# Performance work log

Hardware: AMD Instinct MI355X
Metric: run time of the kernel (lower is better)

## Reference

```python
import jax, jax.numpy as jnp
import numpy as np
import math

THETA = 1.0


def _qdense(xa, xb, wa, wb, ba, bb):
    # QComplexDense: j_squared = -cos(2*theta)
    j2 = -math.cos(2.0 * THETA)
    out_a = xa @ wa.T + j2 * (xb @ wb.T) + ba
    out_b = xa @ wb.T + xb @ wa.T + bb
    return out_a, out_b


def setup_inputs() -> dict:
    key = jax.random.key(0)
    B, S, D = 4, 2048, 1024
    ks = jax.random.split(key, 16)
    limit = math.sqrt(6.0 / (D + D))  # xavier uniform for square [D,D]

    def w(k):
        return jax.random.uniform(k, (D, D), jnp.float32, -limit, limit)

    inp = {
        'xa': jax.random.normal(ks[0], (B, S, D), jnp.float32),
        'xb': jax.random.normal(ks[1], (B, S, D), jnp.float32),
    }
    i = 2
    for n in ('q', 'k', 'v', 'o'):
        inp[n + '_wa'] = w(ks[i]); inp[n + '_wb'] = w(ks[i + 1])
        inp[n + '_ba'] = jnp.zeros((D,), jnp.float32)
        inp[n + '_bb'] = jnp.zeros((D,), jnp.float32)
        i += 2
    return inp


def reference(xa, xb,
              q_wa, q_wb, q_ba, q_bb,
              k_wa, k_wb, k_ba, k_bb,
              v_wa, v_wb, v_ba, v_bb,
              o_wa, o_wb, o_ba, o_bb):
    D = xa.shape[-1]
    # NOTE: qc_matmul in the original uses cos(2 * ones(1)) == cos(2.0),
    # a constant independent of theta.
    c2 = math.cos(2.0)

    Qa, Qb = _qdense(xa, xb, q_wa, q_wb, q_ba, q_bb)
    Ka, Kb = _qdense(xa, xb, k_wa, k_wb, k_ba, k_bb)
    Va, Vb = _qdense(xa, xb, v_wa, v_wb, v_ba, v_bb)

    # complex-style QK^T: scores_a = Qa Ka^T - cos(2) Qb Kb^T ; scores_b = Qa Kb^T + Qb Ka^T
    sa = jnp.einsum('bsd,btd->bst', Qa, Ka) - c2 * jnp.einsum('bsd,btd->bst', Qb, Kb)
    sb = jnp.einsum('bsd,btd->bst', Qa, Kb) + jnp.einsum('bsd,btd->bst', Qb, Ka)
    scores_real = jnp.sqrt(sa * sa + sb * sb)  # magnitude
    attn = jax.nn.softmax(scores_real / math.sqrt(D), axis=-1)  # [B,S,S]

    out_a = jnp.einsum('bst,btd->bsd', attn, Va)
    out_b = jnp.einsum('bst,btd->bsd', attn, Vb)
    return _qdense(out_a, out_b, o_wa, o_wb, o_ba, o_bb)
```

## Files before the change

### kernel.cpp

```cpp
#include <hip/hip_runtime.h>
#include <math.h>

typedef __bf16 bf16_t;
typedef __attribute__((ext_vector_type(16))) float f32x16;
typedef __attribute__((ext_vector_type(8))) __bf16 v8bf;
typedef __attribute__((ext_vector_type(4))) __bf16 v4bf;

#define GLLDS(g, l)                                                           \
  __builtin_amdgcn_global_load_lds(                                           \
      (const __attribute__((address_space(1))) void*)(g),                     \
      (__attribute__((address_space(3))) void*)(l), 16, 0, 0)
#define OPQ(p) asm volatile("" : "+v"(p))

__global__ void sentinel_kernel(float* o, float v) { o[0] = v; }

__global__ __launch_bounds__(256) void pack_x_kernel(
    const float* __restrict__ xa, const float* __restrict__ xb,
    bf16_t* __restrict__ xcat, int n4)
{
  int i = blockIdx.x * 256 + threadIdx.x;
  if (i >= n4) return;
  float4 a = reinterpret_cast<const float4*>(xa)[i];
  float4 b = reinterpret_cast<const float4*>(xb)[i];
  long e = (long)i * 4;
  long m = e >> 10;
  int  d = (int)(e & 1023);
  v4bf av = { (bf16_t)a.x, (bf16_t)a.y, (bf16_t)a.z, (bf16_t)a.w };
  v4bf bv = { (bf16_t)b.x, (bf16_t)b.y, (bf16_t)b.z, (bf16_t)b.w };
  *reinterpret_cast<v4bf*>(xcat + m * 2048 + d)        = av;
  *reinterpret_cast<v4bf*>(xcat + m * 2048 + 1024 + d) = bv;
}

__global__ __launch_bounds__(256) void pack_w_kernel(
    const float* __restrict__ wa, const float* __restrict__ wb,
    bf16_t* __restrict__ outA, bf16_t* __restrict__ outB, float j2)
{
  int i = blockIdx.x * 256 + threadIdx.x;
  float4 a = reinterpret_cast<const float4*>(wa)[i];
  float4 b = reinterpret_cast<const float4*>(wb)[i];
  long e = (long)i * 4;
  long n = e >> 10;
  int  k = (int)(e & 1023);
  v4bf av = { (bf16_t)a.x, (bf16_t)a.y, (bf16_t)a.z, (bf16_t)a.w };
  v4bf bv = { (bf16_t)b.x, (bf16_t)b.y, (bf16_t)b.z, (bf16_t)b.w };
  v4bf jb = { (bf16_t)(j2*b.x), (bf16_t)(j2*b.y), (bf16_t)(j2*b.z), (bf16_t)(j2*b.w) };
  *reinterpret_cast<v4bf*>(outA + n * 2048 + k)        = av;
  *reinterpret_cast<v4bf*>(outA + n * 2048 + 1024 + k) = jb;
  *reinterpret_cast<v4bf*>(outB + n * 2048 + k)        = bv;
  *reinterpret_cast<v4bf*>(outB + n * 2048 + 1024 + k) = av;
}

template<int EPI>
__global__ __launch_bounds__(512) void gemm256_kernel(
    const bf16_t* __restrict__ A, const bf16_t* __restrict__ B,
    int K, long lda, long ldb, long bsA, long bsB,
    void* __restrict__ o0p, void* __restrict__ o1p, void* __restrict__ o2p,
    const float* __restrict__ bb0, const float* __restrict__ bb1,
    const float* __restrict__ bb2, const float* __restrict__ bb3,
    const float* __restrict__ bb4, const float* __restrict__ bb5,
    float scl)
{
  __shared__ __align__(16) bf16_t lds[65536];
  const int tid  = threadIdx.x;
  const int wid  = tid >> 6;
  const int lane = tid & 63;
  const int wm = wid >> 2;
  const int wn = wid & 3;

  const long row0 = (long)blockIdx.y * 256;
  const long col0 = (long)blockIdx.x * 256;
  const int z = blockIdx.z;
  const bf16_t* Ab = A + (long)z * bsA + row0 * lda;
  const bf16_t* Bb = B + (long)z * bsB + col0 * ldb;

  const int srow = wid * 8 + (lane >> 3);
  const int scol = ((lane & 7) ^ (lane >> 3)) * 8;
  const int dbase = wid * 512;

  const bf16_t* sA0 = Ab + (long)srow * lda + scol;
  const bf16_t* sA1 = Ab + (long)(srow + 64) * lda + scol;
  const bf16_t* sA2 = Ab + (long)(srow + 128) * lda + scol;
  const bf16_t* sA3 = Ab + (long)(srow + 192) * lda + scol;
  const bf16_t* sB0 = Bb + (long)srow * ldb + scol;
  const bf16_t* sB1 = Bb + (long)(srow + 64) * ldb + scol;
  const bf16_t* sB2 = Bb + (long)(srow + 128) * ldb + scol;
  const bf16_t* sB3 = Bb + (long)(srow + 192) * ldb + scol;

  const int r32 = lane & 31;
  const int kg2 = lane >> 5;
  const int r7 = r32 & 7;
  const bf16_t *pAs[4], *pBs[4];
#pragma unroll
  for (int s = 0; s < 4; ++s) {
    const int ch = (((kg2 + 2 * s) ^ r7) & 7) * 8;
    pAs[s] = lds + (wm * 128 + r32) * 64 + ch;
    pBs[s] = lds + 16384 + (wn * 64 + r32) * 64 + ch;
  }

  f32x16 acc[4][2];
#pragma unroll
  for (int i = 0; i < 4; ++i)
#pragma unroll
    for (int j = 0; j < 2; ++j)
#pragma unroll
      for (int e = 0; e < 16; ++e) acc[i][j][e] = 0.f;

  const int T = K >> 6;

  GLLDS(sA0, lds + dbase);
  GLLDS(sA1, lds + 4096 + dbase);
  GLLDS(sA2, lds + 8192 + dbase);
  GLLDS(sA3, lds + 12288 + dbase);
  GLLDS(sB0, lds + 16384 + dbase);
  GLLDS(sB1, lds + 16384 + 4096 + dbase);
  GLLDS(sB2, lds + 16384 + 8192 + dbase);
  GLLDS(sB3, lds + 16384 + 12288 + dbase);
  sA0 += 64; sA1 += 64; sA2 += 64; sA3 += 64;
  sB0 += 64; sB1 += 64; sB2 += 64; sB3 += 64;
  OPQ(sA0); OPQ(sA1); OPQ(sA2); OPQ(sA3);
  OPQ(sB0); OPQ(sB1); OPQ(sB2); OPQ(sB3);
  asm volatile("s_waitcnt vmcnt(0)" ::: "memory");
  __builtin_amdgcn_sched_barrier(0);
  __builtin_amdgcn_s_barrier();

#define TILE_BODY(U, PF)                                                       \
  {                                                                            \
    const int so_ = (U) * 32768;                                               \
    const int ns_ = (1 - (U)) * 32768;                                         \
    v8bf a_[4][2], b_[2][2];                                                   \
                                             \
    _Pragma("unroll") for (int g = 0; g < 2; ++g)                              \
      _Pragma("unroll") for (int ss = 0; ss < 2; ++ss)                         \
        b_[g][ss] = *reinterpret_cast<const v8bf*>(pBs[ss] + so_ + g * 2048);  \
    _Pragma("unroll") for (int f = 0; f < 4; ++f)                              \
      _Pragma("unroll") for (int ss = 0; ss < 2; ++ss)                         \
        a_[f][ss] = *reinterpret_cast<const v8bf*>(pAs[ss] + so_ + f * 2048);  \
    if (PF) {                                                                  \
      GLLDS(sA0, lds + ns_ + dbase);                                           \
      GLLDS(sA1, lds + ns_ + 4096 + dbase);                                    \
      GLLDS(sA2, lds + ns_ + 8192 + dbase);                                    \
      GLLDS(sA3, lds + ns_ + 12288 + dbase);                                   \
    }                                                                          \
    __builtin_amdgcn_s_setprio(1);                                             \
    _Pragma("unroll") for (int ss = 0; ss < 2; ++ss)                           \
      _Pragma("unroll") for (int f = 0; f < 4; ++f)                            \
        _Pragma("unroll") for (int g = 0; g < 2; ++g)                          \
          acc[f][g] = __builtin_amdgcn_mfma_f32_32x32x16_bf16(a_[f][ss], b_[g][ss], acc[f][g], 0, 0, 0); \
    __builtin_amdgcn_s_setprio(0);                                             \
                                             \
    _Pragma("unroll") for (int g = 0; g < 2; ++g)                              \
      _Pragma("unroll") for (int ss = 0; ss < 2; ++ss)                         \
        b_[g][ss] = *reinterpret_cast<const v8bf*>(pBs[2 + ss] + so_ + g * 2048); \
    _Pragma("unroll") for (int f = 0; f < 4; ++f)                              \
      _Pragma("unroll") for (int ss = 0; ss < 2; ++ss)                         \
        a_[f][ss] = *reinterpret_cast<const v8bf*>(pAs[2 + ss] + so_ + f * 2048); \
    if (PF) {                                                                  \
      GLLDS(sB0, lds + ns_ + 16384 + dbase);                                   \
      GLLDS(sB1, lds + ns_ + 16384 + 4096 + dbase);                            \
      GLLDS(sB2, lds + ns_ + 16384 + 8192 + dbase);                            \
      GLLDS(sB3, lds + ns_ + 16384 + 12288 + dbase);                           \
      sA0 += 64; sA1 += 64; sA2 += 64; sA3 += 64;                              \
      sB0 += 64; sB1 += 64; sB2 += 64; sB3 += 64;                              \
      OPQ(sA0); OPQ(sA1); OPQ(sA2); OPQ(sA3);                                  \
      OPQ(sB0); OPQ(sB1); OPQ(sB2); OPQ(sB3);                                  \
    }                                                                          \
    __builtin_amdgcn_s_setprio(1);                                             \
    _Pragma("unroll") for (int ss = 0; ss < 2; ++ss)                           \
      _Pragma("unroll") for (int f = 0; f < 4; ++f)                            \
        _Pragma("unroll") for (int g = 0; g < 2; ++g)                          \
          acc[f][g] = __builtin_amdgcn_mfma_f32_32x32x16_bf16(a_[f][ss], b_[g][ss], acc[f][g], 0, 0, 0); \
    __builtin_amdgcn_s_setprio(0);                                             \
    asm volatile("s_waitcnt vmcnt(0)" ::: "memory");                           \
    __builtin_amdgcn_sched_barrier(0);                                         \
    __builtin_amdgcn_s_barrier();                                              \
  }

  for (int tb = 0; tb < T - 2; tb += 2) {
    TILE_BODY(0, 1)
    TILE_BODY(1, 1)
  }
  TILE_BODY(0, 1)
  TILE_BODY(1, 0)
#undef TILE_BODY

  const int hi = lane >> 5;
#pragma unroll
  for (int fm = 0; fm < 4; ++fm) {
#pragma unroll
    for (int fn = 0; fn < 2; ++fn) {
      const f32x16 v = acc[fm][fn];
      const long rowb = row0 + wm * 128 + fm * 32 + 4 * hi;
      const long col  = col0 + wn * 64 + fn * 32 + r32;
      if constexpr (EPI == 0) {
        const int  seg = (int)(col >> 10);
        const long c   = col & 1023;
        bf16_t* Q  = (bf16_t*)o0p;
        bf16_t* Kc = (bf16_t*)o1p;
        bf16_t* Vc = (bf16_t*)o2p;
        switch (seg) {
          case 0: { const float bv = bb0[c];
#pragma unroll
            for (int r = 0; r < 16; ++r) {
              const long row = rowb + (r & 3) + 8 * (r >> 2);
              Q[row * 2048 + c] = (bf16_t)((v[r] + bv) * 0.03125f);
            } } break;
          case 1: { const float bv = bb1[c];
#pragma unroll
            for (int r = 0; r < 16; ++r) {
              const long row = rowb + (r & 3) + 8 * (r >> 2);
              Q[row * 2048 + 1024 + c] = (bf16_t)((v[r] + bv) * 0.03125f);
            } } break;
          case 2: { const float bv = bb2[c];
#pragma unroll
            for (int r = 0; r < 16; ++r) {
              const long row = rowb + (r & 3) + 8 * (r >> 2);
              const long kb2 = (row >> 11) * 8388608 + (row & 2047) * 4096;
              const float w = v[r] + bv;
              Kc[kb2 + c]               = (bf16_t)w;
              Kc[kb2 + 2048 + 1024 + c] = (bf16_t)w;
            } } break;
          case 3: { const float bv = bb3[c];
#pragma unroll
            for (int r = 0; r < 16; ++r) {
              const long row = rowb + (r & 3) + 8 * (r >> 2);
              const long kb2 = (row >> 11) * 8388608 + (row & 2047) * 4096;
              const float w = v[r] + bv;
              Kc[kb2 + 2048 + c] = (bf16_t)w;
              Kc[kb2 + 1024 + c] = (bf16_t)(scl * w);
            } } break;
          case 4: { const float bv = bb4[c];
#pragma unroll
            for (int r = 0; r < 16; ++r) {
              const long row = rowb + (r & 3) + 8 * (r >> 2);
              Vc[row * 2048 + c] = (bf16_t)(v[r] + bv);
            } } break;
          default: { const float bv = bb5[c];
#pragma unroll
            for (int r = 0; r < 16; ++r) {
              const long row = rowb + (r & 3) + 8 * (r >> 2);
              Vc[row * 2048 + 1024 + c] = (bf16_t)(v[r] + bv);
            } } break;
        }
      } else if constexpr (EPI == 1) {
        bf16_t* dst = (bf16_t*)o0p;
        const long tt = col >> 1;
#pragma unroll
        for (int r = 0; r < 16; ++r) {
          const long row = rowb + (r & 3) + 8 * (r >> 2);
          const float x = v[r];
          const float p = __shfl_xor(x, 1);
          const float mg = sqrtf(x * x + p * p);
          if (!(lane & 1))
            dst[(long)z * 4194304 + row * 2048 + tt] = (bf16_t)mg;
        }
      } else if constexpr (EPI == 2) {
#pragma unroll
        for (int r = 0; r < 16; ++r) {
          const long row = rowb + (r & 3) + 8 * (r >> 2);
          ((bf16_t*)o0p)[(long)z * 4194304 + row * 2048 + col] = (bf16_t)v[r];
        }
      } else {
        const int  seg = (int)(col >> 10);
        const long c   = col & 1023;
        float* dst = seg ? (float*)o1p : (float*)o0p;
        const float bv = seg ? bb1[c] : bb0[c];
#pragma unroll
        for (int r = 0; r < 16; ++r) {
          const long row = rowb + (r & 3) + 8 * (r >> 2);
          dst[row * 1024 + c] = v[r] + bv;
        }
      }
    }
  }
}

__global__ __launch_bounds__(256) void transpose_v_kernel(
    const bf16_t* __restrict__ src, bf16_t* __restrict__ dst)
{
  __shared__ bf16_t t[64][65];
  const int tid = threadIdx.x;
  const int off = blockIdx.z * 1024;
  const long c0 = (long)blockIdx.x * 64;
  const long g0 = (long)blockIdx.y * 64;
#pragma unroll
  for (int it = 0; it < 16; ++it) {
    int idx = it * 256 + tid;
    int r = idx >> 6, c = idx & 63;
    t[r][c] = src[(g0 + r) * 2048 + off + c0 + c];
  }
  __syncthreads();
  const long b  = g0 >> 11;
  const long t0 = g0 & 2047;
#pragma unroll
  for (int it = 0; it < 16; ++it) {
    int idx = it * 256 + tid;
    int nr = idx >> 6, tc = idx & 63;
    dst[b * 4194304 + (off + c0 + nr) * 2048 + t0 + tc] = t[tc][nr];
  }
}

__global__ __launch_bounds__(256) void softmax_kernel(
    const bf16_t* __restrict__ mag, bf16_t* __restrict__ attn)
{
  const int tid = threadIdx.x;
  const long base = (long)blockIdx.x * 2048;
  v4bf m0 = *reinterpret_cast<const v4bf*>(mag + base + tid * 4);
  v4bf m1 = *reinterpret_cast<const v4bf*>(mag + base + 1024 + tid * 4);
  float r[8];
#pragma unroll
  for (int k = 0; k < 4; ++k) r[k] = (float)m0[k];
#pragma unroll
  for (int k = 0; k < 4; ++k) r[4 + k] = (float)m1[k];
  float m = r[0];
#pragma unroll
  for (int k = 1; k < 8; ++k) m = fmaxf(m, r[k]);
#pragma unroll
  for (int off = 32; off > 0; off >>= 1) m = fmaxf(m, __shfl_xor(m, off));
  __shared__ float red[8];
  if ((tid & 63) == 0) red[tid >> 6] = m;
  __syncthreads();
  m = fmaxf(fmaxf(red[0], red[1]), fmaxf(red[2], red[3]));
  float p[8], s = 0.f;
#pragma unroll
  for (int k = 0; k < 8; ++k) { p[k] = __expf(r[k] - m); s += p[k]; }
#pragma unroll
  for (int off = 32; off > 0; off >>= 1) s += __shfl_xor(s, off);
  if ((tid & 63) == 0) red[4 + (tid >> 6)] = s;
  __syncthreads();
  const float inv = 1.f / (red[4] + red[5] + red[6] + red[7]);
  v4bf o0 = { (bf16_t)(p[0]*inv), (bf16_t)(p[1]*inv), (bf16_t)(p[2]*inv), (bf16_t)(p[3]*inv) };
  v4bf o1 = { (bf16_t)(p[4]*inv), (bf16_t)(p[5]*inv), (bf16_t)(p[6]*inv), (bf16_t)(p[7]*inv) };
  *reinterpret_cast<v4bf*>(attn + base + tid * 4)        = o0;
  *reinterpret_cast<v4bf*>(attn + base + 1024 + tid * 4) = o1;
}

extern "C" void kernel_launch(void* const* d_in, const int* in_sizes, int n_in,
                              void* d_out, int out_size, void* d_ws, size_t ws_size,
                              hipStream_t stream)
{
  (void)in_sizes; (void)n_in; (void)out_size;
  const float* xa = (const float*)d_in[0];
  const float* xb = (const float*)d_in[1];
  const float *w_a[4], *w_b[4], *b_a[4], *b_b[4];
  for (int p = 0; p < 4; ++p) {
    w_a[p] = (const float*)d_in[2 + p*4 + 0];
    w_b[p] = (const float*)d_in[2 + p*4 + 1];
    b_a[p] = (const float*)d_in[2 + p*4 + 2];
    b_b[p] = (const float*)d_in[2 + p*4 + 3];
  }
  float* out = (float*)d_out;
  const float neg_c2 = (float)(-cos(2.0));

  const size_t WFULL = 33554432ull;
  const size_t WQKV  = 25165824ull;
  int NB = 0; bool fullW = true;
  if      (ws_size >= WFULL + 6ull * 4ull * 8388608ull) NB = 4;
  else if (ws_size >= WFULL + 6ull * 2ull * 8388608ull) NB = 2;
  else if (ws_size >= WFULL + 6ull * 1ull * 8388608ull) NB = 1;
  else if (ws_size >= WQKV  + 6ull * 1ull * 8388608ull) { NB = 1; fullW = false; }
  else { sentinel_kernel<<<1, 1, 0, stream>>>(out, (float)ws_size); return; }

  char* ws = (char*)d_ws;
  const size_t wbytes = fullW ? WFULL : WQKV;
  const size_t RB = (size_t)NB * 8388608ull;
  bf16_t* Wqkv = (bf16_t*)ws;
  bf16_t* Wo   = fullW ? (bf16_t*)(ws + WQKV) : Wqkv;
  bf16_t* R0 = (bf16_t*)(ws + wbytes);
  bf16_t* R1 = (bf16_t*)(ws + wbytes + 1*RB);
  bf16_t* Kc = (bf16_t*)(ws + wbytes + 2*RB);
  bf16_t* R4 = (bf16_t*)(ws + wbytes + 4*RB);
  bf16_t* R5 = (bf16_t*)(ws + wbytes + 5*RB);

  const int  Mc = NB * 2048;
  const dim3 blk(256);
  const dim3 blk512(512);
  const dim3 gqkv(24, Mc / 256, 1);
  const dim3 gsc(16, 8, NB);
  const dim3 gpv(8, 8, NB);
  const dim3 go(8, Mc / 256, 1);
  const dim3 gtr(16, Mc / 64, 2);

  if (fullW) {
    for (int p = 0; p < 3; ++p)
      pack_w_kernel<<<1024, blk, 0, stream>>>(w_a[p], w_b[p],
          Wqkv + (size_t)(2*p)   * 2097152ull,
          Wqkv + (size_t)(2*p+1) * 2097152ull, neg_c2);
    pack_w_kernel<<<1024, blk, 0, stream>>>(w_a[3], w_b[3],
        Wo, Wo + 2097152ull, neg_c2);
  }

  for (int c = 0; c < 4 / NB; ++c) {
    const size_t xoff = (size_t)c * NB * 2097152ull;
    pack_x_kernel<<<Mc, blk, 0, stream>>>(xa + xoff, xb + xoff, R0, Mc * 256);

    if (!fullW)
      for (int p = 0; p < 3; ++p)
        pack_w_kernel<<<1024, blk, 0, stream>>>(w_a[p], w_b[p],
            Wqkv + (size_t)(2*p)   * 2097152ull,
            Wqkv + (size_t)(2*p+1) * 2097152ull, neg_c2);

    gemm256_kernel<0><<<gqkv, blk512, 0, stream>>>(R0, Wqkv, 2048, 2048, 2048, 0, 0,
        R1, Kc, R4, b_a[0], b_b[0], b_a[1], b_b[1], b_a[2], b_b[2], neg_c2);

    transpose_v_kernel<<<gtr, blk, 0, stream>>>(R4, R5);

    gemm256_kernel<1><<<gsc, blk512, 0, stream>>>(R1, Kc, 2048, 2048, 2048, 4194304, 8388608,
        R0, nullptr, nullptr, nullptr, nullptr, nullptr, nullptr, nullptr, nullptr, 0.f);

    softmax_kernel<<<Mc, blk, 0, stream>>>(R0, R0);

    gemm256_kernel<2><<<gpv, blk512, 0, stream>>>(R0, R5, 2048, 2048, 2048, 4194304, 4194304,
        R1, nullptr, nullptr, nullptr, nullptr, nullptr, nullptr, nullptr, nullptr, 0.f);

    if (!fullW)
      pack_w_kernel<<<1024, blk, 0, stream>>>(w_a[3], w_b[3], Wo, Wo + 2097152ull, neg_c2);
    gemm256_kernel<3><<<go, blk512, 0, stream>>>(R1, Wo, 2048, 2048, 2048, 0, 0,
        out + xoff, out + 8388608ull + xoff, nullptr,
        b_a[3], b_b[3], nullptr, nullptr, nullptr, nullptr, 0.f);
  }
}
```

Baseline: 556.6 us.

## Shrink GEMM block tile to 128x256 with K=32 stages and smaller LDS

Reworks the shared GEMM kernel from a 256x256 tile with K-step 64 to a 128x256 tile with K-step 32. LDS use drops from 128KB to 48KB double-buffered, with a new swizzle and load mapping. Each wave now holds a 2x2 accumulator grid instead of 4x2, and grid dimensions double in M. The aim is more resident blocks per CU and better occupancy, at the cost of less operand reuse per tile and more barriers per unit of K.

```diff
diff --git a/kernel.cpp b/kernel.cpp
--- a/kernel.cpp
+++ b/kernel.cpp
@@ -60,115 +60,89 @@
     const float* __restrict__ bb4, const float* __restrict__ bb5,
     float scl)
 {
-  __shared__ __align__(16) bf16_t lds[65536];
+  __shared__ __align__(16) bf16_t lds[24576];
   const int tid  = threadIdx.x;
   const int wid  = tid >> 6;
   const int lane = tid & 63;
   const int wm = wid >> 2;
   const int wn = wid & 3;
 
-  const long row0 = (long)blockIdx.y * 256;
+  const long row0 = (long)blockIdx.y * 128;
   const long col0 = (long)blockIdx.x * 256;
   const int z = blockIdx.z;
   const bf16_t* Ab = A + (long)z * bsA + row0 * lda;
   const bf16_t* Bb = B + (long)z * bsB + col0 * ldb;
 
-  const int srow = wid * 8 + (lane >> 3);
-  const int scol = ((lane & 7) ^ (lane >> 3)) * 8;
+  const int rhat = tid >> 2;
+  const int scol = ((tid & 3) * 8) ^ (((rhat >> 1) & 3) << 3);
   const int dbase = wid * 512;
 
-  const bf16_t* sA0 = Ab + (long)srow * lda + scol;
-  const bf16_t* sA1 = Ab + (long)(srow + 64) * lda + scol;
-  const bf16_t* sA2 = Ab + (long)(srow + 128) * lda + scol;
-  const bf16_t* sA3 = Ab + (long)(srow + 192) * lda + scol;
-  const bf16_t* sB0 = Bb + (long)srow * ldb + scol;
-  const bf16_t* sB1 = Bb + (long)(srow + 64) * ldb + scol;
-  const bf16_t* sB2 = Bb + (long)(srow + 128) * ldb + scol;
-  const bf16_t* sB3 = Bb + (long)(srow + 192) * ldb + scol;
+  const bf16_t* sA0 = Ab + (long)rhat * lda + scol;
+  const bf16_t* sB0 = Bb + (long)rhat * ldb + scol;
+  const bf16_t* sB1 = Bb + (long)(rhat + 128) * ldb + scol;
 
   const int r32 = lane & 31;
   const int kg2 = lane >> 5;
-  const int r7 = r32 & 7;
-  const bf16_t *pAs[4], *pBs[4];
-#pragma unroll
-  for (int s = 0; s < 4; ++s) {
-    const int ch = (((kg2 + 2 * s) ^ r7) & 7) * 8;
-    pAs[s] = lds + (wm * 128 + r32) * 64 + ch;
-    pBs[s] = lds + 16384 + (wn * 64 + r32) * 64 + ch;
-  }
-
-  f32x16 acc[4][2];
-#pragma unroll
-  for (int i = 0; i < 4; ++i)
+  const int kq0 = (kg2 * 8) ^ ((((r32 >> 1) & 3)) << 3);
+  const bf16_t* pA0 = lds + (wm * 64 + r32) * 32 + kq0;
+  const bf16_t* pA1 = lds + (wm * 64 + r32) * 32 + (kq0 ^ 16);
+  const bf16_t* pB0 = lds + 4096 + (wn * 64 + r32) * 32 + kq0;
+  const bf16_t* pB1 = lds + 4096 + (wn * 64 + r32) * 32 + (kq0 ^ 16);
+
+  f32x16 acc[2][2];
+#pragma unroll
+  for (int i = 0; i < 2; ++i)
 #pragma unroll
     for (int j = 0; j < 2; ++j)
 #pragma unroll
       for (int e = 0; e < 16; ++e) acc[i][j][e] = 0.f;
 
-  const int T = K >> 6;
+  const int T = K >> 5;
 
   GLLDS(sA0, lds + dbase);
-  GLLDS(sA1, lds + 4096 + dbase);
-  GLLDS(sA2, lds + 8192 + dbase);
-  GLLDS(sA3, lds + 12288 + dbase);
-  GLLDS(sB0, lds + 16384 + dbase);
-  GLLDS(sB1, lds + 16384 + 4096 + dbase);
-  GLLDS(sB2, lds + 16384 + 8192 + dbase);
-  GLLDS(sB3, lds + 16384 + 12288 + dbase);
-  sA0 += 64; sA1 += 64; sA2 += 64; sA3 += 64;
-  sB0 += 64; sB1 += 64; sB2 += 64; sB3 += 64;
-  OPQ(sA0); OPQ(sA1); OPQ(sA2); OPQ(sA3);
-  OPQ(sB0); OPQ(sB1); OPQ(sB2); OPQ(sB3);
+  GLLDS(sB0, lds + 4096 + dbase);
+  GLLDS(sB1, lds + 8192 + dbase);
+  sA0 += 32; sB0 += 32; sB1 += 32;
+  OPQ(sA0); OPQ(sB0); OPQ(sB1);
   asm volatile("s_waitcnt vmcnt(0)" ::: "memory");
   __builtin_amdgcn_sched_barrier(0);
   __builtin_amdgcn_s_barrier();
 
 #define TILE_BODY(U, PF)                                                       \
   {                                                                            \
-    const int so_ = (U) * 32768;                                               \
-    const int ns_ = (1 - (U)) * 32768;                                         \
-    v8bf a_[4][2], b_[2][2];                                                   \
-                                             \
-    _Pragma("unroll") for (int g = 0; g < 2; ++g)                              \
-      _Pragma("unroll") for (int ss = 0; ss < 2; ++ss)                         \
-        b_[g][ss] = *reinterpret_cast<const v8bf*>(pBs[ss] + so_ + g * 2048);  \
-    _Pragma("unroll") for (int f = 0; f < 4; ++f)                              \
-      _Pragma("unroll") for (int ss = 0; ss < 2; ++ss)                         \
-        a_[f][ss] = *reinterpret_cast<const v8bf*>(pAs[ss] + so_ + f * 2048);  \
+    const int so_ = (U) * 12288;                                               \
+    const int ns_ = (1 - (U)) * 12288;                                         \
+    v8bf a0_, a1_, b0_, b1_;                                                   \
+                                                            \
+    b0_ = *reinterpret_cast<const v8bf*>(pB0 + so_);                           \
+    b1_ = *reinterpret_cast<const v8bf*>(pB0 + so_ + 1024);                    \
+    a0_ = *reinterpret_cast<const v8bf*>(pA0 + so_);                           \
+    a1_ = *reinterpret_cast<const v8bf*>(pA0 + so_ + 1024);                    \
     if (PF) {                                                                  \
       GLLDS(sA0, lds + ns_ + dbase);                                           \
-      GLLDS(sA1, lds + ns_ + 4096 + dbase);                                    \
-      GLLDS(sA2, lds + ns_ + 8192 + dbase);                                    \
-      GLLDS(sA3, lds + ns_ + 12288 + dbase);                                   \
+      GLLDS(sB0, lds + ns_ + 4096 + dbase);                                    \
+      GLLDS(sB1, lds + ns_ + 8192 + dbase);                                    \
     }                                                                          \
     __builtin_amdgcn_s_setprio(1);                                             \
-    _Pragma("unroll") for (int ss = 0; ss < 2; ++ss)                           \
-      _Pragma("unroll") for (int f = 0; f < 4; ++f)                            \
-        _Pragma("unroll") for (int g = 0; g < 2; ++g)                          \
-          acc[f][g] = __builtin_amdgcn_mfma_f32_32x32x16_bf16(a_[f][ss], b_[g][ss], acc[f][g], 0, 0, 0); \
+    acc[0][0] = __builtin_amdgcn_mfma_f32_32x32x16_bf16(a0_, b0_, acc[0][0], 0, 0, 0); \
+    acc[0][1] = __builtin_amdgcn_mfma_f32_32x32x16_bf16(a0_, b1_, acc[0][1], 0, 0, 0); \
+    acc[1][0] = __builtin_amdgcn_mfma_f32_32x32x16_bf16(a1_, b0_, acc[1][0], 0, 0, 0); \
+    acc[1][1] = __builtin_amdgcn_mfma_f32_32x32x16_bf16(a1_, b1_, acc[1][1], 0, 0, 0); \
     __builtin_amdgcn_s_setprio(0);                                             \
-                                             \
-    _Pragma("unroll") for (int g = 0; g < 2; ++g)                              \
-      _Pragma("unroll") for (int ss = 0; ss < 2; ++ss)                         \
-        b_[g][ss] = *reinterpret_cast<const v8bf*>(pBs[2 + ss] + so_ + g * 2048); \
-    _Pragma("unroll") for (int f = 0; f < 4; ++f)                              \
-      _Pragma("unroll") for (int ss = 0; ss < 2; ++ss)                         \
-        a_[f][ss] = *reinterpret_cast<const v8bf*>(pAs[2 + ss] + so_ + f * 2048); \
+                                                            \
+    b0_ = *reinterpret_cast<const v8bf*>(pB1 + so_);                           \
+    b1_ = *reinterpret_cast<const v8bf*>(pB1 + so_ + 1024);                    \
+    a0_ = *reinterpret_cast<const v8bf*>(pA1 + so_);                           \
+    a1_ = *reinterpret_cast<const v8bf*>(pA1 + so_ + 1024);                    \
     if (PF) {                                                                  \
-      GLLDS(sB0, lds + ns_ + 16384 + dbase);                                   \
-      GLLDS(sB1, lds + ns_ + 16384 + 4096 + dbase);                            \
-      GLLDS(sB2, lds + ns_ + 16384 + 8192 + dbase);                            \
-      GLLDS(sB3, lds + ns_ + 16384 + 12288 + dbase);                           \
-      sA0 += 64; sA1 += 64; sA2 += 64; sA3 += 64;                              \
-      sB0 += 64; sB1 += 64; sB2 += 64; sB3 += 64;                              \
-      OPQ(sA0); OPQ(sA1); OPQ(sA2); OPQ(sA3);                                  \
-      OPQ(sB0); OPQ(sB1); OPQ(sB2); OPQ(sB3);                                  \
+      sA0 += 32; sB0 += 32; sB1 += 32;                                         \
+      OPQ(sA0); OPQ(sB0); OPQ(sB1);                                            \
     }                                                                          \
     __builtin_amdgcn_s_setprio(1);                                             \
-    _Pragma("unroll") for (int ss = 0; ss < 2; ++ss)                           \
-      _Pragma("unroll") for (int f = 0; f < 4; ++f)                            \
-        _Pragma("unroll") for (int g = 0; g < 2; ++g)                          \
-          acc[f][g] = __builtin_amdgcn_mfma_f32_32x32x16_bf16(a_[f][ss], b_[g][ss], acc[f][g], 0, 0, 0); \
+    acc[0][0] = __builtin_amdgcn_mfma_f32_32x32x16_bf16(a0_, b0_, acc[0][0], 0, 0, 0); \
+    acc[0][1] = __builtin_amdgcn_mfma_f32_32x32x16_bf16(a0_, b1_, acc[0][1], 0, 0, 0); \
+    acc[1][0] = __builtin_amdgcn_mfma_f32_32x32x16_bf16(a1_, b0_, acc[1][0], 0, 0, 0); \
+    acc[1][1] = __builtin_amdgcn_mfma_f32_32x32x16_bf16(a1_, b1_, acc[1][1], 0, 0, 0); \
     __builtin_amdgcn_s_setprio(0);                                             \
     asm volatile("s_waitcnt vmcnt(0)" ::: "memory");                           \
     __builtin_amdgcn_sched_barrier(0);                                         \
@@ -185,11 +159,11 @@
 
   const int hi = lane >> 5;
 #pragma unroll
-  for (int fm = 0; fm < 4; ++fm) {
+  for (int fm = 0; fm < 2; ++fm) {
 #pragma unroll
     for (int fn = 0; fn < 2; ++fn) {
       const f32x16 v = acc[fm][fn];
-      const long rowb = row0 + wm * 128 + fm * 32 + 4 * hi;
+      const long rowb = row0 + wm * 64 + fm * 32 + 4 * hi;
       const long col  = col0 + wn * 64 + fn * 32 + r32;
       if constexpr (EPI == 0) {
         const int  seg = (int)(col >> 10);
@@ -374,10 +348,10 @@
   const int  Mc = NB * 2048;
   const dim3 blk(256);
   const dim3 blk512(512);
-  const dim3 gqkv(24, Mc / 256, 1);
-  const dim3 gsc(16, 8, NB);
-  const dim3 gpv(8, 8, NB);
-  const dim3 go(8, Mc / 256, 1);
+  const dim3 gqkv(24, Mc / 128, 1);
+  const dim3 gsc(16, 16, NB);
+  const dim3 gpv(8, 16, NB);
+  const dim3 go(8, Mc / 128, 1);
   const dim3 gtr(16, Mc / 64, 2);
 
   if (fullW) {
```

Measured after the change: 618.1 us. +11.0%, slower.

## Use 4-wave GEMM blocks with 128x128 per-wave tiles

Applied to the files above, without the earlier changes.

Changes the 256x256 GEMM from 8 waves (each computing 128x64) to 4 waves (each computing 128x128), doubling the accumulators per wave and reorganizing the LDS fragment reads and MFMA schedule. Each wave now issues twice as many global-to-LDS loads per tile. The aim is more data reuse per fragment read and fewer LDS reads per MFMA. In exchange, register pressure rises sharply (256 accumulator VGPRs) and fewer waves are available to hide latency.

```diff
diff --git a/kernel.cpp b/kernel.cpp
--- a/kernel.cpp
+++ b/kernel.cpp
@@ -51,7 +51,7 @@
 }
 
 template<int EPI>
-__global__ __launch_bounds__(512) void gemm256_kernel(
+__global__ __launch_bounds__(256) void gemm256_kernel(
     const bf16_t* __restrict__ A, const bf16_t* __restrict__ B,
     int K, long lda, long ldb, long bsA, long bsB,
     void* __restrict__ o0p, void* __restrict__ o1p, void* __restrict__ o2p,
@@ -64,8 +64,8 @@
   const int tid  = threadIdx.x;
   const int wid  = tid >> 6;
   const int lane = tid & 63;
-  const int wm = wid >> 2;
-  const int wn = wid & 3;
+  const int wm = wid >> 1;
+  const int wn = wid & 1;
 
   const long row0 = (long)blockIdx.y * 256;
   const long col0 = (long)blockIdx.x * 256;
@@ -77,99 +77,82 @@
   const int scol = ((lane & 7) ^ (lane >> 3)) * 8;
   const int dbase = wid * 512;
 
-  const bf16_t* sA0 = Ab + (long)srow * lda + scol;
-  const bf16_t* sA1 = Ab + (long)(srow + 64) * lda + scol;
-  const bf16_t* sA2 = Ab + (long)(srow + 128) * lda + scol;
-  const bf16_t* sA3 = Ab + (long)(srow + 192) * lda + scol;
-  const bf16_t* sB0 = Bb + (long)srow * ldb + scol;
-  const bf16_t* sB1 = Bb + (long)(srow + 64) * ldb + scol;
-  const bf16_t* sB2 = Bb + (long)(srow + 128) * ldb + scol;
-  const bf16_t* sB3 = Bb + (long)(srow + 192) * ldb + scol;
+  const bf16_t *sA[8], *sB[8];
+#pragma unroll
+  for (int i = 0; i < 8; ++i) {
+    sA[i] = Ab + (long)(srow + 32 * i) * lda + scol;
+    sB[i] = Bb + (long)(srow + 32 * i) * ldb + scol;
+  }
 
   const int r32 = lane & 31;
   const int kg2 = lane >> 5;
   const int r7 = r32 & 7;
-  const bf16_t *pAs[4], *pBs[4];
+  const bf16_t *pA[4], *pB[4];
 #pragma unroll
   for (int s = 0; s < 4; ++s) {
     const int ch = (((kg2 + 2 * s) ^ r7) & 7) * 8;
-    pAs[s] = lds + (wm * 128 + r32) * 64 + ch;
-    pBs[s] = lds + 16384 + (wn * 64 + r32) * 64 + ch;
-  }
-
-  f32x16 acc[4][2];
+    pA[s] = lds + (wm * 128 + r32) * 64 + ch;
+    pB[s] = lds + 16384 + (wn * 128 + r32) * 64 + ch;
+  }
+
+  f32x16 acc[4][4];
 #pragma unroll
   for (int i = 0; i < 4; ++i)
 #pragma unroll
-    for (int j = 0; j < 2; ++j)
+    for (int j = 0; j < 4; ++j)
 #pragma unroll
       for (int e = 0; e < 16; ++e) acc[i][j][e] = 0.f;
 
   const int T = K >> 6;
 
-  GLLDS(sA0, lds + dbase);
-  GLLDS(sA1, lds + 4096 + dbase);
-  GLLDS(sA2, lds + 8192 + dbase);
-  GLLDS(sA3, lds + 12288 + dbase);
-  GLLDS(sB0, lds + 16384 + dbase);
-  GLLDS(sB1, lds + 16384 + 4096 + dbase);
-  GLLDS(sB2, lds + 16384 + 8192 + dbase);
-  GLLDS(sB3, lds + 16384 + 12288 + dbase);
-  sA0 += 64; sA1 += 64; sA2 += 64; sA3 += 64;
-  sB0 += 64; sB1 += 64; sB2 += 64; sB3 += 64;
-  OPQ(sA0); OPQ(sA1); OPQ(sA2); OPQ(sA3);
-  OPQ(sB0); OPQ(sB1); OPQ(sB2); OPQ(sB3);
+#pragma unroll
+  for (int i = 0; i < 8; ++i) GLLDS(sA[i], lds + i * 2048 + dbase);
+#pragma unroll
+  for (int i = 0; i < 8; ++i) GLLDS(sB[i], lds + 16384 + i * 2048 + dbase);
+#pragma unroll
+  for (int i = 0; i < 8; ++i) { sA[i] += 64; sB[i] += 64; OPQ(sA[i]); OPQ(sB[i]); }
   asm volatile("s_waitcnt vmcnt(0)" ::: "memory");
   __builtin_amdgcn_sched_barrier(0);
   __builtin_amdgcn_s_barrier();
+
+#define RD(dst, base, so_)                                                     \
+    _Pragma("unroll") for (int f = 0; f < 4; ++f)                              \
+      dst[f] = *reinterpret_cast<const v8bf*>((base) + (so_) + f * 2048);
+
+#define MM(af, bf)                                                             \
+    __builtin_amdgcn_s_setprio(1);                                             \
+    _Pragma("unroll") for (int f = 0; f < 4; ++f)                              \
+      _Pragma("unroll") for (int g = 0; g < 4; ++g)                            \
+        acc[f][g] = __builtin_amdgcn_mfma_f32_32x32x16_bf16(af[f], bf[g], acc[f][g], 0, 0, 0); \
+    __builtin_amdgcn_s_setprio(0);
 
 #define TILE_BODY(U, PF)                                                       \
   {                                                                            \
     const int so_ = (U) * 32768;                                               \
     const int ns_ = (1 - (U)) * 32768;                                         \
-    v8bf a_[4][2], b_[2][2];                                                   \
-                                             \
-    _Pragma("unroll") for (int g = 0; g < 2; ++g)                              \
-      _Pragma("unroll") for (int ss = 0; ss < 2; ++ss)                         \
-        b_[g][ss] = *reinterpret_cast<const v8bf*>(pBs[ss] + so_ + g * 2048);  \
-    _Pragma("unroll") for (int f = 0; f < 4; ++f)                              \
-      _Pragma("unroll") for (int ss = 0; ss < 2; ++ss)                         \
-        a_[f][ss] = *reinterpret_cast<const v8bf*>(pAs[ss] + so_ + f * 2048);  \
+    v8bf a0_[4], b0_[4], a1_[4], b1_[4];                                       \
+    RD(b0_, pB[0], so_) RD(a0_, pA[0], so_)                                    \
+                               \
+    RD(b1_, pB[1], so_) RD(a1_, pA[1], so_)                                    \
     if (PF) {                                                                  \
-      GLLDS(sA0, lds + ns_ + dbase);                                           \
-      GLLDS(sA1, lds + ns_ + 4096 + dbase);                                    \
-      GLLDS(sA2, lds + ns_ + 8192 + dbase);                                    \
-      GLLDS(sA3, lds + ns_ + 12288 + dbase);                                   \
+      _Pragma("unroll") for (int i = 0; i < 8; ++i)                            \
+        GLLDS(sA[i], lds + ns_ + i * 2048 + dbase);                            \
     }                                                                          \
-    __builtin_amdgcn_s_setprio(1);                                             \
-    _Pragma("unroll") for (int ss = 0; ss < 2; ++ss)                           \
-      _Pragma("unroll") for (int f = 0; f < 4; ++f)                            \
-        _Pragma("unroll") for (int g = 0; g < 2; ++g)                          \
-          acc[f][g] = __builtin_amdgcn_mfma_f32_32x32x16_bf16(a_[f][ss], b_[g][ss], acc[f][g], 0, 0, 0); \
-    __builtin_amdgcn_s_setprio(0);                                             \
-                                             \
-    _Pragma("unroll") for (int g = 0; g < 2; ++g)                              \
-      _Pragma("unroll") for (int ss = 0; ss < 2; ++ss)                         \
-        b_[g][ss] = *reinterpret_cast<const v8bf*>(pBs[2 + ss] + so_ + g * 2048); \
-    _Pragma("unroll") for (int f = 0; f < 4; ++f)                              \
-      _Pragma("unroll") for (int ss = 0; ss < 2; ++ss)                         \
-        a_[f][ss] = *reinterpret_cast<const v8bf*>(pAs[2 + ss] + so_ + f * 2048); \
+    MM(a0_, b0_)                                                               \
+                               \
+    RD(b0_, pB[2], so_) RD(a0_, pA[2], so_)                                    \
     if (PF) {                                                                  \
-      GLLDS(sB0, lds + ns_ + 16384 + dbase);                                   \
-      GLLDS(sB1, lds + ns_ + 16384 + 4096 + dbase);                            \
-      GLLDS(sB2, lds + ns_ + 16384 + 8192 + dbase);                            \
-      GLLDS(sB3, lds + ns_ + 16384 + 12288 + dbase);                           \
-      sA0 += 64; sA1 += 64; sA2 += 64; sA3 += 64;                              \
-      sB0 += 64; sB1 += 64; sB2 += 64; sB3 += 64;                              \
-      OPQ(sA0); OPQ(sA1); OPQ(sA2); OPQ(sA3);                                  \
-      OPQ(sB0); OPQ(sB1); OPQ(sB2); OPQ(sB3);                                  \
+      _Pragma("unroll") for (int i = 0; i < 8; ++i)                            \
+        GLLDS(sB[i], lds + ns_ + 16384 + i * 2048 + dbase);                    \
+      _Pragma("unroll") for (int i = 0; i < 8; ++i)                            \
+        { sA[i] += 64; sB[i] += 64; OPQ(sA[i]); OPQ(sB[i]); }                  \
     }                                                                          \
-    __builtin_amdgcn_s_setprio(1);                                             \
-    _Pragma("unroll") for (int ss = 0; ss < 2; ++ss)                           \
-      _Pragma("unroll") for (int f = 0; f < 4; ++f)                            \
-        _Pragma("unroll") for (int g = 0; g < 2; ++g)                          \
-          acc[f][g] = __builtin_amdgcn_mfma_f32_32x32x16_bf16(a_[f][ss], b_[g][ss], acc[f][g], 0, 0, 0); \
-    __builtin_amdgcn_s_setprio(0);                                             \
+    MM(a1_, b1_)                                                               \
+                                        \
+    RD(b1_, pB[3], so_) RD(a1_, pA[3], so_)                                    \
+    MM(a0_, b0_)                                                               \
+                                                                  \
+    MM(a1_, b1_)                                                               \
     asm volatile("s_waitcnt vmcnt(0)" ::: "memory");                           \
     __builtin_amdgcn_sched_barrier(0);                                         \
     __builtin_amdgcn_s_barrier();                                              \
@@ -182,15 +165,17 @@
   TILE_BODY(0, 1)
   TILE_BODY(1, 0)
 #undef TILE_BODY
+#undef RD
+#undef MM
 
   const int hi = lane >> 5;
 #pragma unroll
   for (int fm = 0; fm < 4; ++fm) {
 #pragma unroll
-    for (int fn = 0; fn < 2; ++fn) {
+    for (int fn = 0; fn < 4; ++fn) {
       const f32x16 v = acc[fm][fn];
       const long rowb = row0 + wm * 128 + fm * 32 + 4 * hi;
-      const long col  = col0 + wn * 64 + fn * 32 + r32;
+      const long col  = col0 + wn * 128 + fn * 32 + r32;
       if constexpr (EPI == 0) {
         const int  seg = (int)(col >> 10);
         const long c   = col & 1023;
@@ -373,7 +358,6 @@
 
   const int  Mc = NB * 2048;
   const dim3 blk(256);
-  const dim3 blk512(512);
   const dim3 gqkv(24, Mc / 256, 1);
   const dim3 gsc(16, 8, NB);
   const dim3 gpv(8, 8, NB);
@@ -399,22 +383,22 @@
             Wqkv + (size_t)(2*p)   * 2097152ull,
             Wqkv + (size_t)(2*p+1) * 2097152ull, neg_c2);
 
-    gemm256_kernel<0><<<gqkv, blk512, 0, stream>>>(R0, Wqkv, 2048, 2048, 2048, 0, 0,
+    gemm256_kernel<0><<<gqkv, blk, 0, stream>>>(R0, Wqkv, 2048, 2048, 2048, 0, 0,
         R1, Kc, R4, b_a[0], b_b[0], b_a[1], b_b[1], b_a[2], b_b[2], neg_c2);
 
     transpose_v_kernel<<<gtr, blk, 0, stream>>>(R4, R5);
 
-    gemm256_kernel<1><<<gsc, blk512, 0, stream>>>(R1, Kc, 2048, 2048, 2048, 4194304, 8388608,
+    gemm256_kernel<1><<<gsc, blk, 0, stream>>>(R1, Kc, 2048, 2048, 2048, 4194304, 8388608,
         R0, nullptr, nullptr, nullptr, nullptr, nullptr, nullptr, nullptr, nullptr, 0.f);
 
     softmax_kernel<<<Mc, blk, 0, stream>>>(R0, R0);
 
-    gemm256_kernel<2><<<gpv, blk512, 0, stream>>>(R0, R5, 2048, 2048, 2048, 4194304, 4194304,
+    gemm256_kernel<2><<<gpv, blk, 0, stream>>>(R0, R5, 2048, 2048, 2048, 4194304, 4194304,
         R1, nullptr, nullptr, nullptr, nullptr, nullptr, nullptr, nullptr, nullptr, 0.f);
 
     if (!fullW)
       pack_w_kernel<<<1024, blk, 0, stream>>>(w_a[3], w_b[3], Wo, Wo + 2097152ull, neg_c2);
-    gemm256_kernel<3><<<go, blk512, 0, stream>>>(R1, Wo, 2048, 2048, 2048, 0, 0,
+    gemm256_kernel<3><<<go, blk, 0, stream>>>(R1, Wo, 2048, 2048, 2048, 0, 0,
         out + xoff, out + 8388608ull + xoff, nullptr,
         b_a[3], b_b[3], nullptr, nullptr, nullptr, nullptr, 0.f);
   }
```

New measurement: 610.6 us. +9.7%, slower.
